# Performance work log

Measured on AMD Instinct MI355X. Metric: run time of the kernel, lower is better.

Reference implementation:

```python
import jax, jax.numpy as jnp
import numpy as np

D, H, DK, DF = 512, 8, 64, 2048  # dim, heads, head_dim, forward_dim
EPS = 1e-5


def _layernorm(x, g, b):
    mu = jnp.mean(x, axis=-1, keepdims=True)
    var = jnp.mean(jnp.square(x - mu), axis=-1, keepdims=True)
    return (x - mu) * jax.lax.rsqrt(var + EPS) * g + b


def setup_inputs() -> dict:
    key = jax.random.key(0)
    ks = jax.random.split(key, 16)
    B, S = 2, 2048
    s_in = 1.0 / np.sqrt(D)
    s_ff = 1.0 / np.sqrt(DF)
    s_cat = 1.0 / np.sqrt(H * DK)
    return {
        "x": jax.random.normal(ks[0], (B, S, D), jnp.float32),
        # per-head Q/K/V projections stacked over heads: [H, D, DK]
        "Wq": jax.random.uniform(ks[1], (H, D, DK), jnp.float32, -s_in, s_in),
        "bq": jax.random.uniform(ks[2], (H, DK), jnp.float32, -s_in, s_in),
        "Wk": jax.random.uniform(ks[3], (H, D, DK), jnp.float32, -s_in, s_in),
        "bk": jax.random.uniform(ks[4], (H, DK), jnp.float32, -s_in, s_in),
        "Wv": jax.random.uniform(ks[5], (H, D, DK), jnp.float32, -s_in, s_in),
        "bv": jax.random.uniform(ks[6], (H, DK), jnp.float32, -s_in, s_in),
        "Wo": jax.random.uniform(ks[7], (H * DK, D), jnp.float32, -s_cat, s_cat),
        "bo": jax.random.uniform(ks[8], (D,), jnp.float32, -s_cat, s_cat),
        "ln1_g": jnp.ones((D,), jnp.float32),
        "ln1_b": jnp.zeros((D,), jnp.float32),
        "W1": jax.random.uniform(ks[9], (D, DF), jnp.float32, -s_in, s_in),
        "b1": jax.random.uniform(ks[10], (DF,), jnp.float32, -s_in, s_in),
        "W2": jax.random.uniform(ks[11], (DF, D), jnp.float32, -s_ff, s_ff),
        "b2": jax.random.uniform(ks[12], (D,), jnp.float32, -s_ff, s_ff),
        "ln2_g": jnp.ones((D,), jnp.float32),
        "ln2_b": jnp.zeros((D,), jnp.float32),
    }


def reference(x, Wq, bq, Wk, bk, Wv, bv, Wo, bo, ln1_g, ln1_b, W1, b1, W2, b2, ln2_g, ln2_b):
    # Per-head projections, batched over heads: [B,H,S,DK]
    q = jnp.einsum('bsd,hdk->bhsk', x, Wq) + bq[None, :, None, :]
    k = jnp.einsum('bsd,hdk->bhsk', x, Wk) + bk[None, :, None, :]
    v = jnp.einsum('bsd,hdk->bhsk', x, Wv) + bv[None, :, None, :]
    scale = 1.0 / np.sqrt(DK)
    scores = jnp.einsum('bhsk,bhtk->bhst', q, k) * scale  # [B,H,S,S]
    attn = jax.nn.softmax(scores, axis=-1)
    o = jnp.einsum('bhst,bhtk->bhsk', attn, v)  # [B,H,S,DK]
    # concat heads (head order matches torch cat over ModuleList)
    B, _, S, _ = o.shape
    o = o.transpose(0, 2, 1, 3).reshape(B, S, H * DK)
    attn_out = o @ Wo + bo
    # Residual 1 (dropout = identity in eval): LN(x + sublayer(x))
    h = _layernorm(x + attn_out, ln1_g, ln1_b)
    # FeedForward + Residual 2
    ff = jax.nn.relu(h @ W1 + b1) @ W2 + b2
    return _layernorm(h + ff, ln2_g, ln2_b)
```

## Files before the change

### kernel.cpp

```cpp
#include <hip/hip_runtime.h>


#define Dm   512
#define Hh   8
#define DKk  64
#define DFf  2048
#define Bb   2
#define Ss   2048
#define Nn   4096

typedef __attribute__((ext_vector_type(8))) short short8;
typedef __attribute__((ext_vector_type(4))) float f32x4;
typedef __attribute__((ext_vector_type(4))) short short4v;
typedef __attribute__((ext_vector_type(2))) int   int2v;

__device__ inline float bf2f(short s) {
    unsigned u = ((unsigned)(unsigned short)s) << 16;
    float f; __builtin_memcpy(&f, &u, 4); return f;
}
__device__ inline short f2bf(float f) {
    unsigned u; __builtin_memcpy(&u, &f, 4);
    u = (u + 0x7fff + ((u >> 16) & 1)) >> 16;
    return (short)u;
}
__device__ inline short cvt_elem(const void* p, long i, int f32flag) {
    if (f32flag) return f2bf(((const float*)p)[i]);
    return ((const short*)p)[i];
}
__device__ inline int detect_f32(const void* x) {
    const float* xf = (const float*)x;
    int ok = 0;
#pragma unroll
    for (int i = 0; i < 16; ++i) {
        float a = fabsf(xf[i]);
        ok += (a > 1e-8f && a < 1e4f) ? 1 : 0;
    }
    return ok >= 8;
}
__device__ inline void gload_lds16(const short* g, short* l) {
    __builtin_amdgcn_global_load_lds(
        (const __attribute__((address_space(1))) unsigned int*)g,
        (__attribute__((address_space(3))) unsigned int*)l, 16, 0, 0);
}

__global__ __launch_bounds__(256) void prep_kernel(
    const void* __restrict__ x, short* __restrict__ xb,
    const void* bq, const void* bk, const void* bv, const void* bo,
    const void* b1, const void* b2, const void* g1, const void* be1,
    const void* g2, const void* be2, short* __restrict__ smalls,
    const void* Wq, const void* Wk, const void* Wv,
    const void* Wo, const void* W1, const void* W2,
    short* __restrict__ WqkvT,
    short* __restrict__ WoT, short* __restrict__ W1T, short* __restrict__ W2T)
{
    const int f = detect_f32(x);
    int blk = blockIdx.x;
    if (blk < 512) {
        long base = (long)blk * 4096;
        if (!f) {
            const short8* src8 = (const short8*)((const short*)x + base);
            short8* dst8 = (short8*)(xb + base);
            for (int i = threadIdx.x; i < 512; i += 256) dst8[i] = src8[i];
        } else {
            for (int i = threadIdx.x; i < 4096; i += 256)
                xb[base + i] = cvt_elem(x, base + i, f);
        }
        return;
    }
    if (blk == 512) {
        const void* srcs[10] = {bq, bk, bv, bo, b1, b2, g1, be1, g2, be2};
        const int   sz[10]   = {512, 512, 512, 512, 2048, 512, 512, 512, 512, 512};
        int off = 0;
        for (int j = 0; j < 10; ++j) {
            for (int i = threadIdx.x; i < sz[j]; i += 256)
                smalls[off + i] = cvt_elem(srcs[j], i, f);
            off += sz[j];
        }
        return;
    }
    __shared__ short tile[64][65];
    blk -= 513;
    const void* src; short* dst; long srcoff = 0; long dstoff = 0; int R, C, tr, tc;
    if (blk < 192) {
        int m = blk >> 6; int r = blk & 63; int h = r >> 3; int t = r & 7;
        src = (m == 0) ? Wq : (m == 1) ? Wk : Wv;
        dst = WqkvT + (long)m * 512 * 512;
        srcoff = (long)h * 512 * 64; dstoff = (long)h * 64 * 512;
        R = 512; C = 64; tr = t; tc = 0;
    } else if (blk < 256) {
        int r = blk - 192; src = Wo; dst = WoT; R = 512; C = 512; tr = r >> 3; tc = r & 7;
    } else if (blk < 512) {
        int r = blk - 256; src = W1; dst = W1T; R = 512; C = 2048; tr = r >> 5; tc = r & 31;
    } else {
        int r = blk - 512; src = W2; dst = W2T; R = 2048; C = 512; tr = r >> 3; tc = r & 7;
    }
    int r0 = tr * 64, c0 = tc * 64;
    if (!f) {
        const short* s16 = (const short*)src;
        for (int i = threadIdx.x; i < 512; i += 256) {
            int rr = i >> 3, c8 = (i & 7) * 8;
            short8 v = *(const short8*)&s16[srcoff + (long)(r0 + rr) * C + c0 + c8];
#pragma unroll
            for (int j = 0; j < 8; ++j) tile[rr][c8 + j] = v[j];
        }
        __syncthreads();
        for (int i = threadIdx.x; i < 512; i += 256) {
            int cc = i >> 3, r8 = (i & 7) * 8;
            short8 w;
#pragma unroll
            for (int j = 0; j < 8; ++j) w[j] = tile[r8 + j][cc];
            *(short8*)&dst[dstoff + (long)(c0 + cc) * R + r0 + r8] = w;
        }
    } else {
        for (int i = threadIdx.x; i < 4096; i += 256) {
            int rr = i >> 6, cc = i & 63;
            tile[rr][cc] = cvt_elem(src, srcoff + (long)(r0 + rr) * C + c0 + cc, f);
        }
        __syncthreads();
        for (int i = threadIdx.x; i < 4096; i += 256) {
            int cc = i >> 6, rr = i & 63;
            dst[dstoff + (long)(c0 + cc) * R + r0 + rr] = tile[rr][cc];
        }
    }
}

#define MODE_F32       1
#define MODE_RELU_BF16 2
#define MODE_QKV       4

__global__ __launch_bounds__(256) void gemm_kernel(
    const short* __restrict__ A, const short* __restrict__ Bt,
    const short* __restrict__ bias, void* __restrict__ outp,
    void* __restrict__ out2, void* __restrict__ out3,
    int K, int Ncols, int mode, int Ktile)
{
    __shared__ short As[2][128 * 64];
    __shared__ short Bs[2][128 * 64];
    const int t    = threadIdx.x;
    const int lane = t & 63;
    const int wave = t >> 6;
    const int quad = lane >> 4;
    const int l15  = lane & 15;
    const int wm = wave >> 1, wn = wave & 1;
    const int row0 = blockIdx.x * 128;
    const int col0 = blockIdx.y * 128;
    const int kbase = blockIdx.z * Ktile;

    const int ri = lane >> 3;
    const int ct = (lane & 7) ^ ri;

    f32x4 acc[4][4];
#pragma unroll
    for (int i = 0; i < 4; ++i)
#pragma unroll
        for (int j = 0; j < 4; ++j) acc[i][j] = (f32x4){0.f, 0.f, 0.f, 0.f};

    auto stage = [&](int buf, int k0) {
#pragma unroll
        for (int p = 0; p < 4; ++p) {
            int r = wave * 32 + p * 8;
            gload_lds16(A + (long)(row0 + r + ri) * K + kbase + k0 + ct * 8,
                        &As[buf][r * 64 + lane * 8]);
        }
#pragma unroll
        for (int p = 0; p < 4; ++p) {
            int r = wave * 32 + p * 8;
            gload_lds16(Bt + (long)(col0 + r + ri) * K + kbase + k0 + ct * 8,
                        &Bs[buf][r * 64 + lane * 8]);
        }
    };

    stage(0, 0);
    int cur = 0;
    const int niter = Ktile >> 6;
    for (int it = 0; it < niter; ++it) {
        asm volatile("s_waitcnt vmcnt(0)" ::: "memory");
        __syncthreads();
        if (it + 1 < niter) stage(cur ^ 1, (it + 1) * 64);
#pragma unroll
        for (int kk = 0; kk < 2; ++kk) {
            short8 af[4], bfr[4];
#pragma unroll
            for (int mt = 0; mt < 4; ++mt) {
                int rowa = wm * 64 + mt * 16 + l15;
                af[mt] = *(const short8*)&As[cur][rowa * 64
                              + (((kk * 4 + quad) ^ (rowa & 7)) * 8)];
            }
#pragma unroll
            for (int nt = 0; nt < 4; ++nt) {
                int rowb = wn * 64 + nt * 16 + l15;
                bfr[nt] = *(const short8*)&Bs[cur][rowb * 64
                              + (((kk * 4 + quad) ^ (rowb & 7)) * 8)];
            }
#pragma unroll
            for (int mt = 0; mt < 4; ++mt)
#pragma unroll
                for (int nt = 0; nt < 4; ++nt)
                    acc[mt][nt] = __builtin_amdgcn_mfma_f32_16x16x32_bf16(
                        af[mt], bfr[nt], acc[mt][nt], 0, 0, 0);
        }
        cur ^= 1;
    }

    const int wrow0 = row0 + wm * 64;
    const int wcol0 = col0 + wn * 64;
    if (mode == MODE_QKV) {
        if (wcol0 < 1024) {
            int m = wcol0 >> 9;
            short* out = (short*)(m == 0 ? outp : out2);
            float sc = (m == 0) ? 0.125f : 1.0f;
#pragma unroll
            for (int nt = 0; nt < 4; ++nt) {
                int col = wcol0 + nt * 16 + l15;
                float bb = bf2f(bias[col]);
                int cl = col & 511;
#pragma unroll
                for (int mt = 0; mt < 4; ++mt)
#pragma unroll
                    for (int r = 0; r < 4; ++r) {
                        int row = wrow0 + mt * 16 + quad * 4 + r;
                        out[(long)row * 512 + cl] = f2bf((acc[mt][nt][r] + bb) * sc);
                    }
            }
        } else {
            __syncthreads();
            short* Asf = &As[0][0];
#pragma unroll
            for (int nt = 0; nt < 4; ++nt) {
                int col_l = wn * 64 + nt * 16 + l15;
                float bb = bf2f(bias[col0 + col_l]);
#pragma unroll
                for (int mt = 0; mt < 4; ++mt) {
                    int row4 = wm * 16 + mt * 4 + quad;
                    int slot = row4 ^ (col_l & 31);
                    short4v pk;
#pragma unroll
                    for (int r = 0; r < 4; ++r) pk[r] = f2bf(acc[mt][nt][r] + bb);
                    *(short4v*)&Asf[col_l * 128 + slot * 4] = pk;
                }
            }
            __syncthreads();
            short* out = (short*)out3;
            int col_l = t >> 1;
            int cl = col0 + col_l - 1024;
            int hh = cl >> 6, kk2 = cl & 63;
            int bg = row0 >> 11;
            long obase = ((long)(bg * Hh + hh) * DKk + kk2) * Ss + (row0 & 2047);
#pragma unroll
            for (int i = 0; i < 8; ++i) {
                int chunk = (t & 1) * 8 + i;
                int s0 = (chunk * 2)     ^ (col_l & 31);
                int s1 = (chunk * 2 + 1) ^ (col_l & 31);
                short4v a = *(const short4v*)&Asf[col_l * 128 + s0 * 4];
                short4v b4 = *(const short4v*)&Asf[col_l * 128 + s1 * 4];
                short8 w;
                w[0] = a[0];  w[1] = a[1];  w[2] = a[2];  w[3] = a[3];
                w[4] = b4[0]; w[5] = b4[1]; w[6] = b4[2]; w[7] = b4[3];
                *(short8*)&out[obase + chunk * 8] = w;
            }
        }
    } else if (mode == MODE_F32) {
        float* out = (float*)outp + (long)blockIdx.z * Nn * Ncols;
        int zb = (blockIdx.z == 0);
#pragma unroll
        for (int nt = 0; nt < 4; ++nt) {
            int col = wcol0 + nt * 16 + l15;
            float bb = zb ? bf2f(bias[col]) : 0.f;
#pragma unroll
            for (int mt = 0; mt < 4; ++mt)
#pragma unroll
                for (int r = 0; r < 4; ++r) {
                    int row = wrow0 + mt * 16 + quad * 4 + r;
                    out[(long)row * Ncols + col] = acc[mt][nt][r] + bb;
                }
        }
    } else {
        short* out = (short*)outp;
#pragma unroll
        for (int nt = 0; nt < 4; ++nt) {
            int col = wcol0 + nt * 16 + l15;
            float bb = bf2f(bias[col]);
#pragma unroll
            for (int mt = 0; mt < 4; ++mt)
#pragma unroll
                for (int r = 0; r < 4; ++r) {
                    int row = wrow0 + mt * 16 + quad * 4 + r;
                    out[(long)row * Ncols + col] = f2bf(fmaxf(acc[mt][nt][r] + bb, 0.f));
                }
        }
    }
}

__global__ __launch_bounds__(256) void wogemm_kernel(
    const short* __restrict__ po, const float* __restrict__ ls,
    const short* __restrict__ Bt, const short* __restrict__ bias,
    float* __restrict__ outp)
{
    __shared__ short As[2][128 * 64];
    __shared__ short Bs[2][128 * 64];
    const int t    = threadIdx.x;
    const int lane = t & 63;
    const int wave = t >> 6;
    const int quad = lane >> 4;
    const int l15  = lane & 15;
    const int wm = wave >> 1, wn = wave & 1;
    const int row0 = blockIdx.x * 128;
    const int col0 = blockIdx.y * 128;
    const int z    = blockIdx.z;

    const int ri = lane >> 3;
    const int ct = (lane & 7) ^ ri;
    const int myrow = t >> 1;
    const int tcb = (t & 1) * 4;
    const int bg = row0 >> 11;
    const int qtl = (row0 >> 7) & 15;

    f32x4 acc[4][4];
#pragma unroll
    for (int i = 0; i < 4; ++i)
#pragma unroll
        for (int j = 0; j < 4; ++j) acc[i][j] = (f32x4){0.f, 0.f, 0.f, 0.f};

    auto stageB = [&](int buf, int k0) {
#pragma unroll
        for (int p = 0; p < 4; ++p) {
            int r = wave * 32 + p * 8;
            gload_lds16(Bt + (long)(col0 + r + ri) * 512 + z * 256 + k0 + ct * 8,
                        &Bs[buf][r * 64 + lane * 8]);
        }
    };

    short8 aR[4][4];
    float  lR[4];
    auto loadA = [&](int it) {
        int h = z * 4 + it;
        long pbase = ((long)(bg * Hh + h) * 16 + qtl) * 4;
#pragma unroll
        for (int ks = 0; ks < 4; ++ks) {
            lR[ks] = ls[(pbase + ks) * 128 + myrow];
#pragma unroll
            for (int c = 0; c < 4; ++c)
                aR[c][ks] = *(const short8*)&po[((pbase + ks) * 128 + myrow) * 64
                                                + (tcb + c) * 8];
        }
    };
    auto cvtwrite = [&](int buf) {
        float invL = __builtin_amdgcn_rcpf(lR[0] + lR[1] + lR[2] + lR[3]);
#pragma unroll
        for (int c = 0; c < 4; ++c) {
            short8 w;
#pragma unroll
            for (int j = 0; j < 8; ++j) {
                float s = bf2f(aR[c][0][j]) + bf2f(aR[c][1][j])
                        + bf2f(aR[c][2][j]) + bf2f(aR[c][3][j]);
                w[j] = f2bf(s * invL);
            }
            int slot = (tcb + c) ^ (myrow & 7);
            *(short8*)&As[buf][myrow * 64 + slot * 8] = w;
        }
    };

    loadA(0); stageB(0, 0); cvtwrite(0);
    int cur = 0;
#pragma unroll
    for (int it = 0; it < 4; ++it) {
        __syncthreads();
        if (it < 3) { loadA(it + 1); stageB(cur ^ 1, (it + 1) * 64); }
#pragma unroll
        for (int kk = 0; kk < 2; ++kk) {
            short8 af[4], bfr[4];
#pragma unroll
            for (int mt = 0; mt < 4; ++mt) {
                int rowa = wm * 64 + mt * 16 + l15;
                af[mt] = *(const short8*)&As[cur][rowa * 64
                              + (((kk * 4 + quad) ^ (rowa & 7)) * 8)];
            }
#pragma unroll
            for (int nt = 0; nt < 4; ++nt) {
                int rowb = wn * 64 + nt * 16 + l15;
                bfr[nt] = *(const short8*)&Bs[cur][rowb * 64
                              + (((kk * 4 + quad) ^ (rowb & 7)) * 8)];
            }
#pragma unroll
            for (int mt = 0; mt < 4; ++mt)
#pragma unroll
                for (int nt = 0; nt < 4; ++nt)
                    acc[mt][nt] = __builtin_amdgcn_mfma_f32_16x16x32_bf16(
                        af[mt], bfr[nt], acc[mt][nt], 0, 0, 0);
        }
        if (it < 3) cvtwrite(cur ^ 1);
        cur ^= 1;
    }

    const int wrow0 = row0 + wm * 64;
    const int wcol0 = col0 + wn * 64;
    float* out = outp + (long)z * Nn * Dm;
    int zb = (z == 0);
#pragma unroll
    for (int nt = 0; nt < 4; ++nt) {
        int col = wcol0 + nt * 16 + l15;
        float bb = zb ? bf2f(bias[col]) : 0.f;
#pragma unroll
        for (int mt = 0; mt < 4; ++mt)
#pragma unroll
            for (int r = 0; r < 4; ++r) {
                int row = wrow0 + mt * 16 + quad * 4 + r;
                out[(long)row * Dm + col] = acc[mt][nt][r] + bb;
            }
    }
}

__global__ __launch_bounds__(256) void attn_kernel(
    const short* __restrict__ Q, const short* __restrict__ Kt,
    const short* __restrict__ Vt, short* __restrict__ po, float* __restrict__ ls)
{
    __shared__ __align__(16) short Ks[64 * 64];
    __shared__ __align__(16) short Vs[64 * 64];
    __shared__ __align__(16) short pbuf[4][32 * 72];
    const int lane = threadIdx.x & 63;
    const int wave = threadIdx.x >> 6;
    const int quad = lane >> 4;
    const int l15  = lane & 15;
    const int qt = blockIdx.x, bh = blockIdx.y, ks = blockIdx.z;
    const int b = bh >> 3, h = bh & 7;
    const int qrow = b * Ss + qt * 128 + wave * 32;

    short8 bq[2][2];
#pragma unroll
    for (int qh = 0; qh < 2; ++qh)
#pragma unroll
        for (int kk = 0; kk < 2; ++kk)
            bq[qh][kk] = *(const short8*)(Q + (long)(qrow + qh * 16 + l15) * Dm
                                          + h * DKk + kk * 32 + quad * 8);

    f32x4 o[2][4];
    float lsum[2] = {0.f, 0.f};
#pragma unroll
    for (int qh = 0; qh < 2; ++qh)
#pragma unroll
        for (int nt = 0; nt < 4; ++nt) o[qh][nt] = (f32x4){0.f, 0.f, 0.f, 0.f};

    const short* Kg = Kt + (long)b * Ss * Dm + h * DKk;
    const short* Vg = Vt + (long)bh * DKk * Ss;
    short* pbw = pbuf[wave];
    const int t00 = ks * 512;

    const int ri = lane >> 3;
    const int ct = (lane & 7) ^ ri;
    const int ldsrow0 = wave * 16;

    for (int it = 0; it < 8; ++it) {
        const int t0 = t00 + it * 64;
#pragma unroll
        for (int p = 0; p < 2; ++p) {
            int r = ldsrow0 + p * 8 + ri;
            gload_lds16(Kg + (long)(t0 + r) * Dm + ct * 8,
                        &Ks[(ldsrow0 + p * 8) * 64] + lane * 8);
        }
#pragma unroll
        for (int p = 0; p < 2; ++p) {
            int r = ldsrow0 + p * 8 + ri;
            gload_lds16(Vg + (long)r * Ss + t0 + ct * 8,
                        &Vs[(ldsrow0 + p * 8) * 64] + lane * 8);
        }
        asm volatile("s_waitcnt vmcnt(0)" ::: "memory");
        __syncthreads();

#pragma unroll
        for (int j = 0; j < 4; ++j) {
            short8 kf0 = *(const short8*)&Ks[(j * 16 + l15) * 64
                                             + ((quad ^ (l15 & 7)) * 8)];
            short8 kf1 = *(const short8*)&Ks[(j * 16 + l15) * 64
                                             + (((4 + quad) ^ (l15 & 7)) * 8)];
#pragma unroll
            for (int qh = 0; qh < 2; ++qh) {
                f32x4 sj = (f32x4){0.f, 0.f, 0.f, 0.f};
                sj = __builtin_amdgcn_mfma_f32_16x16x32_bf16(kf0, bq[qh][0], sj, 0, 0, 0);
                sj = __builtin_amdgcn_mfma_f32_16x16x32_bf16(kf1, bq[qh][1], sj, 0, 0, 0);
                int2v pk;
#pragma unroll
                for (int r2 = 0; r2 < 2; ++r2) {
                    float pa = __expf(fminf(sj[r2 * 2 + 0], 20.f));
                    float pc = __expf(fminf(sj[r2 * 2 + 1], 20.f));
                    lsum[qh] += pa + pc;
                    unsigned ua, uc;
                    __builtin_memcpy(&ua, &pa, 4);
                    __builtin_memcpy(&uc, &pc, 4);
                    pk[r2] = __builtin_amdgcn_perm(uc, ua, 0x07060302);
                }
                *(int2v*)&pbw[(qh * 16 + l15) * 72 + j * 16 + quad * 4] = pk;
            }
        }
        asm volatile("s_waitcnt lgkmcnt(0)" ::: "memory");
#pragma unroll
        for (int c = 0; c < 2; ++c) {
            short8 ap[2];
#pragma unroll
            for (int qh = 0; qh < 2; ++qh)
                ap[qh] = *(const short8*)&pbw[(qh * 16 + l15) * 72 + c * 32 + quad * 8];
#pragma unroll
            for (int nt = 0; nt < 4; ++nt) {
                short8 vf = *(const short8*)&Vs[(nt * 16 + l15) * 64
                                                + (((c * 4 + quad) ^ (l15 & 7)) * 8)];
#pragma unroll
                for (int qh = 0; qh < 2; ++qh)
                    o[qh][nt] = __builtin_amdgcn_mfma_f32_16x16x32_bf16(
                        ap[qh], vf, o[qh][nt], 0, 0, 0);
            }
        }
        asm volatile("" ::: "memory");
        __syncthreads();
    }

#pragma unroll
    for (int qh = 0; qh < 2; ++qh) {
        float v = lsum[qh];
        v += __shfl_xor(v, 16);
        v += __shfl_xor(v, 32);
        lsum[qh] = v;
    }
    short* pob = po + ((((long)bh * 16 + qt) * 4 + ks) * 128) * 64;
#pragma unroll
    for (int qh = 0; qh < 2; ++qh)
#pragma unroll
        for (int nt = 0; nt < 4; ++nt)
#pragma unroll
            for (int r = 0; r < 4; ++r)
                pob[(wave * 32 + qh * 16 + quad * 4 + r) * 64 + nt * 16 + l15] =
                    f2bf(o[qh][nt][r]);
    if (lane < 16) {
        long lbase = (((long)bh * 16 + qt) * 4 + ks) * 128 + wave * 32;
        ls[lbase + l15]      = lsum[0];
        ls[lbase + 16 + l15] = lsum[1];
    }
}

__global__ __launch_bounds__(256) void ln_kernel(
    const float* __restrict__ v0, const float* __restrict__ v1,
    const float* __restrict__ v2, const float* __restrict__ v3,
    const short* __restrict__ res,
    const short* __restrict__ g, const short* __restrict__ bt,
    void* __restrict__ out, const void* __restrict__ xdet)
{
    const int row = blockIdx.x, tid = threadIdx.x;
    const long base = (long)row * Dm;
    const long i0 = base + tid, i1 = base + 256 + tid;
    float x0 = v0[i0] + bf2f(res[i0]);
    float x1 = v0[i1] + bf2f(res[i1]);
    if (v1) { x0 += v1[i0]; x1 += v1[i1]; }
    if (v2) { x0 += v2[i0]; x1 += v2[i1]; }
    if (v3) { x0 += v3[i0]; x1 += v3[i1]; }

    __shared__ float red[8];
    const int wv = tid >> 6, ln = tid & 63;
    float s = x0 + x1;
#pragma unroll
    for (int mk = 1; mk < 64; mk <<= 1) s += __shfl_xor(s, mk);
    if (!ln) red[wv] = s;
    __syncthreads();
    float mean = (red[0] + red[1] + red[2] + red[3]) * (1.f / 512.f);
    float d0 = x0 - mean, d1 = x1 - mean;
    float q = d0 * d0 + d1 * d1;
#pragma unroll
    for (int mk = 1; mk < 64; mk <<= 1) q += __shfl_xor(q, mk);
    if (!ln) red[4 + wv] = q;
    __syncthreads();
    float rs = rsqrtf((red[4] + red[5] + red[6] + red[7]) * (1.f / 512.f) + 1e-5f);
    float y0 = d0 * rs * bf2f(g[tid])       + bf2f(bt[tid]);
    float y1 = d1 * rs * bf2f(g[256 + tid]) + bf2f(bt[256 + tid]);
    int f32out = xdet ? detect_f32(xdet) : 0;
    if (f32out) {
        float* o = (float*)out;
        o[i0] = y0; o[i1] = y1;
    } else {
        short* o = (short*)out;
        o[i0] = f2bf(y0); o[i1] = f2bf(y1);
    }
}

extern "C" void kernel_launch(void* const* d_in, const int* in_sizes, int n_in,
                              void* d_out, int out_size, void* d_ws, size_t ws_size,
                              hipStream_t stream)
{
    (void)in_sizes; (void)n_in; (void)out_size; (void)ws_size;
    const void* x   = d_in[0];
    const void* Wq  = d_in[1];  const void* bq  = d_in[2];
    const void* Wk  = d_in[3];  const void* bk  = d_in[4];
    const void* Wv  = d_in[5];  const void* bv  = d_in[6];
    const void* Wo  = d_in[7];  const void* bo  = d_in[8];
    const void* g1  = d_in[9];  const void* be1 = d_in[10];
    const void* W1  = d_in[11]; const void* b1  = d_in[12];
    const void* W2  = d_in[13]; const void* b2  = d_in[14];
    const void* g2  = d_in[15]; const void* be2 = d_in[16];

    char* ws = (char*)d_ws;
    size_t off = 0;
    auto alloc = [&](size_t bytes) -> void* {
        void* p = ws + off; off += (bytes + 255) & ~(size_t)255; return p;
    };
    short* WqkvT = (short*)alloc((size_t)3 * Dm * Dm * 2);
    short* WoT   = (short*)alloc((size_t)Dm * Dm * 2);
    short* W1T   = (short*)alloc((size_t)DFf * Dm * 2);
    short* W2T   = (short*)alloc((size_t)Dm * DFf * 2);
    short* xb    = (short*)alloc((size_t)Nn * Dm * 2);
    short* sm    = (short*)alloc((size_t)6656 * 2);
    char*  regA  = (char*)alloc((size_t)Nn * DFf * 2);
    short* Qb    = (short*)(regA);
    short* Kb    = (short*)(regA + (size_t)Nn * Dm * 2);
    short* Vt    = (short*)(regA + (size_t)Nn * Dm * 4);
    short* u     = (short*)(regA);
    float* wo_p  = (float*)alloc((size_t)2 * Nn * Dm * 4);
    char*  regC  = (char*)alloc((size_t)4 * Nn * Dm * 4);
    short* po    = (short*)regC;
    float* f2p   = (float*)regC;
    float* lsb   = (float*)alloc((size_t)16 * 16 * 4 * 128 * 4);
    short* h_bf  = (short*)alloc((size_t)Nn * Dm * 2);

    prep_kernel<<<1281, 256, 0, stream>>>(x, xb, bq, bk, bv, bo, b1, b2,
                                          g1, be1, g2, be2, sm,
                                          Wq, Wk, Wv, Wo, W1, W2,
                                          WqkvT, WoT, W1T, W2T);
    gemm_kernel<<<dim3(Nn / 128, 1536 / 128, 1), 256, 0, stream>>>(
        xb, WqkvT, sm + 0, Qb, Kb, Vt, Dm, 1536, MODE_QKV, Dm);
    attn_kernel<<<dim3(Ss / 128, Bb * Hh, 4), 256, 0, stream>>>(Qb, Kb, Vt, po, lsb);
    wogemm_kernel<<<dim3(Nn / 128, Dm / 128, 2), 256, 0, stream>>>(
        po, lsb, WoT, sm + 1536, wo_p);
    ln_kernel<<<Nn, 256, 0, stream>>>(wo_p, wo_p + (long)Nn * Dm, nullptr, nullptr,
                                      xb, sm + 4608, sm + 5120, h_bf, nullptr);
    gemm_kernel<<<dim3(Nn / 128, DFf / 128, 1), 256, 0, stream>>>(
        h_bf, W1T, sm + 2048, u, nullptr, nullptr, Dm, DFf, MODE_RELU_BF16, Dm);
    gemm_kernel<<<dim3(Nn / 128, Dm / 128, 4), 256, 0, stream>>>(
        u, W2T, sm + 4096, f2p, nullptr, nullptr, DFf, Dm, MODE_F32, DFf / 4);
    ln_kernel<<<Nn, 256, 0, stream>>>(f2p, f2p + (long)Nn * Dm, f2p + (long)2 * Nn * Dm,
                                      f2p + (long)3 * Nn * Dm,
                                      h_bf, sm + 5632, sm + 6144, d_out, x);
}
```

Baseline: 209.4 us.

## Stage GEMM epilogues through LDS and store split-K partials as bf16

Adds a shared epilogue helper that writes each accumulator tile into LDS and then emits coalesced 16-byte row stores. It replaces the scattered 2-byte and 4-byte per-element global stores in the QKV, FFN, Wo and attention output paths. Split-K partial sums for the Wo and W2 GEMMs are now stored as bf16 instead of fp32, which halves the partial-buffer traffic read back by the layernorm kernels. The cost is extra LDS round trips and syncs per tile, plus some loss of precision in the partial sums.

```diff
diff --git a/kernel.cpp b/kernel.cpp
--- a/kernel.cpp
+++ b/kernel.cpp
@@ -41,6 +41,35 @@
     __builtin_amdgcn_global_load_lds(
         (const __attribute__((address_space(1))) unsigned int*)g,
         (__attribute__((address_space(3))) unsigned int*)l, 16, 0, 0);
+}
+
+__device__ inline void epi_store128(
+    short* SM, const f32x4 (&acc)[4][4], const short* bias, int colbias,
+    short* out, long rowbase, long pitch, int colbase,
+    float scale, int relu, int wm, int wn, int quad, int l15, int t)
+{
+    __syncthreads();
+#pragma unroll
+    for (int nt = 0; nt < 4; ++nt) {
+        int col_l = wn * 64 + nt * 16 + l15;
+        float bb = bias ? bf2f(bias[colbias + col_l]) : 0.f;
+#pragma unroll
+        for (int mt = 0; mt < 4; ++mt)
+#pragma unroll
+            for (int r = 0; r < 4; ++r) {
+                int row_l = wm * 64 + mt * 16 + quad * 4 + r;
+                float v = (acc[mt][nt][r] + bb) * scale;
+                if (relu) v = fmaxf(v, 0.f);
+                SM[row_l * 136 + col_l] = f2bf(v);
+            }
+    }
+    __syncthreads();
+    int row_l = t >> 1;
+    int x0 = (t & 1) * 64;
+#pragma unroll
+    for (int k = 0; k < 8; ++k)
+        *(short8*)&out[(rowbase + row_l) * pitch + colbase + x0 + k * 8] =
+            *(const short8*)&SM[row_l * 136 + x0 + k * 8];
 }
 
 __global__ __launch_bounds__(256) void prep_kernel(
@@ -124,7 +153,7 @@
     }
 }
 
-#define MODE_F32       1
+#define MODE_PART      1
 #define MODE_RELU_BF16 2
 #define MODE_QKV       4
 
@@ -134,8 +163,9 @@
     void* __restrict__ out2, void* __restrict__ out3,
     int K, int Ncols, int mode, int Ktile)
 {
-    __shared__ short As[2][128 * 64];
-    __shared__ short Bs[2][128 * 64];
+    __shared__ __align__(16) short SMEM[32768];
+    short* As = SMEM;
+    short* Bs = SMEM + 16384;
     const int t    = threadIdx.x;
     const int lane = t & 63;
     const int wave = t >> 6;
@@ -160,13 +190,13 @@
         for (int p = 0; p < 4; ++p) {
             int r = wave * 32 + p * 8;
             gload_lds16(A + (long)(row0 + r + ri) * K + kbase + k0 + ct * 8,
-                        &As[buf][r * 64 + lane * 8]);
+                        &As[buf * 8192 + r * 64 + lane * 8]);
         }
 #pragma unroll
         for (int p = 0; p < 4; ++p) {
             int r = wave * 32 + p * 8;
             gload_lds16(Bt + (long)(col0 + r + ri) * K + kbase + k0 + ct * 8,
-                        &Bs[buf][r * 64 + lane * 8]);
+                        &Bs[buf * 8192 + r * 64 + lane * 8]);
         }
     };
 
@@ -183,13 +213,13 @@
 #pragma unroll
             for (int mt = 0; mt < 4; ++mt) {
                 int rowa = wm * 64 + mt * 16 + l15;
-                af[mt] = *(const short8*)&As[cur][rowa * 64
+                af[mt] = *(const short8*)&As[cur * 8192 + rowa * 64
                               + (((kk * 4 + quad) ^ (rowa & 7)) * 8)];
             }
 #pragma unroll
             for (int nt = 0; nt < 4; ++nt) {
                 int rowb = wn * 64 + nt * 16 + l15;
-                bfr[nt] = *(const short8*)&Bs[cur][rowb * 64
+                bfr[nt] = *(const short8*)&Bs[cur * 8192 + rowb * 64
                               + (((kk * 4 + quad) ^ (rowb & 7)) * 8)];
             }
 #pragma unroll
@@ -202,29 +232,16 @@
         cur ^= 1;
     }
 
-    const int wrow0 = row0 + wm * 64;
-    const int wcol0 = col0 + wn * 64;
     if (mode == MODE_QKV) {
-        if (wcol0 < 1024) {
-            int m = wcol0 >> 9;
+        if (col0 < 1024) {
+            int m = col0 >> 9;
             short* out = (short*)(m == 0 ? outp : out2);
             float sc = (m == 0) ? 0.125f : 1.0f;
-#pragma unroll
-            for (int nt = 0; nt < 4; ++nt) {
-                int col = wcol0 + nt * 16 + l15;
-                float bb = bf2f(bias[col]);
-                int cl = col & 511;
-#pragma unroll
-                for (int mt = 0; mt < 4; ++mt)
-#pragma unroll
-                    for (int r = 0; r < 4; ++r) {
-                        int row = wrow0 + mt * 16 + quad * 4 + r;
-                        out[(long)row * 512 + cl] = f2bf((acc[mt][nt][r] + bb) * sc);
-                    }
-            }
+            epi_store128(SMEM, acc, bias, col0, out, row0, 512, col0 & 511,
+                         sc, 0, wm, wn, quad, l15, t);
         } else {
             __syncthreads();
-            short* Asf = &As[0][0];
+            short* Asf = SMEM;
 #pragma unroll
             for (int nt = 0; nt < 4; ++nt) {
                 int col_l = wn * 64 + nt * 16 + l15;
@@ -259,45 +276,24 @@
                 *(short8*)&out[obase + chunk * 8] = w;
             }
         }
-    } else if (mode == MODE_F32) {
-        float* out = (float*)outp + (long)blockIdx.z * Nn * Ncols;
-        int zb = (blockIdx.z == 0);
-#pragma unroll
-        for (int nt = 0; nt < 4; ++nt) {
-            int col = wcol0 + nt * 16 + l15;
-            float bb = zb ? bf2f(bias[col]) : 0.f;
-#pragma unroll
-            for (int mt = 0; mt < 4; ++mt)
-#pragma unroll
-                for (int r = 0; r < 4; ++r) {
-                    int row = wrow0 + mt * 16 + quad * 4 + r;
-                    out[(long)row * Ncols + col] = acc[mt][nt][r] + bb;
-                }
-        }
+    } else if (mode == MODE_PART) {
+        short* out = (short*)outp + (long)blockIdx.z * Nn * Ncols;
+        epi_store128(SMEM, acc, (blockIdx.z == 0) ? bias : nullptr, col0,
+                     out, row0, Ncols, col0, 1.f, 0, wm, wn, quad, l15, t);
     } else {
-        short* out = (short*)outp;
-#pragma unroll
-        for (int nt = 0; nt < 4; ++nt) {
-            int col = wcol0 + nt * 16 + l15;
-            float bb = bf2f(bias[col]);
-#pragma unroll
-            for (int mt = 0; mt < 4; ++mt)
-#pragma unroll
-                for (int r = 0; r < 4; ++r) {
-                    int row = wrow0 + mt * 16 + quad * 4 + r;
-                    out[(long)row * Ncols + col] = f2bf(fmaxf(acc[mt][nt][r] + bb, 0.f));
-                }
-        }
+        epi_store128(SMEM, acc, bias, col0, (short*)outp, row0, Ncols, col0,
+                     1.f, 1, wm, wn, quad, l15, t);
     }
 }
 
 __global__ __launch_bounds__(256) void wogemm_kernel(
     const short* __restrict__ po, const float* __restrict__ ls,
     const short* __restrict__ Bt, const short* __restrict__ bias,
-    float* __restrict__ outp)
+    short* __restrict__ outp)
 {
-    __shared__ short As[2][128 * 64];
-    __shared__ short Bs[2][128 * 64];
+    __shared__ __align__(16) short SMEM[32768];
+    short* As = SMEM;
+    short* Bs = SMEM + 16384;
     const int t    = threadIdx.x;
     const int lane = t & 63;
     const int wave = t >> 6;
@@ -326,7 +322,7 @@
         for (int p = 0; p < 4; ++p) {
             int r = wave * 32 + p * 8;
             gload_lds16(Bt + (long)(col0 + r + ri) * 512 + z * 256 + k0 + ct * 8,
-                        &Bs[buf][r * 64 + lane * 8]);
+                        &Bs[buf * 8192 + r * 64 + lane * 8]);
         }
     };
 
@@ -356,7 +352,7 @@
                 w[j] = f2bf(s * invL);
             }
             int slot = (tcb + c) ^ (myrow & 7);
-            *(short8*)&As[buf][myrow * 64 + slot * 8] = w;
+            *(short8*)&As[buf * 8192 + myrow * 64 + slot * 8] = w;
         }
     };
 
@@ -372,13 +368,13 @@
 #pragma unroll
             for (int mt = 0; mt < 4; ++mt) {
                 int rowa = wm * 64 + mt * 16 + l15;
-                af[mt] = *(const short8*)&As[cur][rowa * 64
+                af[mt] = *(const short8*)&As[cur * 8192 + rowa * 64
                               + (((kk * 4 + quad) ^ (rowa & 7)) * 8)];
             }
 #pragma unroll
             for (int nt = 0; nt < 4; ++nt) {
                 int rowb = wn * 64 + nt * 16 + l15;
-                bfr[nt] = *(const short8*)&Bs[cur][rowb * 64
+                bfr[nt] = *(const short8*)&Bs[cur * 8192 + rowb * 64
                               + (((kk * 4 + quad) ^ (rowb & 7)) * 8)];
             }
 #pragma unroll
@@ -392,22 +388,9 @@
         cur ^= 1;
     }
 
-    const int wrow0 = row0 + wm * 64;
-    const int wcol0 = col0 + wn * 64;
-    float* out = outp + (long)z * Nn * Dm;
-    int zb = (z == 0);
-#pragma unroll
-    for (int nt = 0; nt < 4; ++nt) {
-        int col = wcol0 + nt * 16 + l15;
-        float bb = zb ? bf2f(bias[col]) : 0.f;
-#pragma unroll
-        for (int mt = 0; mt < 4; ++mt)
-#pragma unroll
-            for (int r = 0; r < 4; ++r) {
-                int row = wrow0 + mt * 16 + quad * 4 + r;
-                out[(long)row * Dm + col] = acc[mt][nt][r] + bb;
-            }
-    }
+    short* out = outp + (long)z * Nn * Dm;
+    epi_store128(SMEM, acc, (z == 0) ? bias : nullptr, col0,
+                 out, row0, Dm, col0, 1.f, 0, wm, wn, quad, l15, t);
 }
 
 __global__ __launch_bounds__(256) void attn_kernel(
@@ -519,15 +502,25 @@
         v += __shfl_xor(v, 32);
         lsum[qh] = v;
     }
+    short* SM = &pbuf[0][0];
+#pragma unroll
+    for (int qh = 0; qh < 2; ++qh)
+#pragma unroll
+        for (int nt = 0; nt < 4; ++nt)
+#pragma unroll
+            for (int r = 0; r < 4; ++r)
+                SM[(wave * 32 + qh * 16 + quad * 4 + r) * 72 + nt * 16 + l15] =
+                    f2bf(o[qh][nt][r]);
+    __syncthreads();
     short* pob = po + ((((long)bh * 16 + qt) * 4 + ks) * 128) * 64;
-#pragma unroll
-    for (int qh = 0; qh < 2; ++qh)
-#pragma unroll
-        for (int nt = 0; nt < 4; ++nt)
-#pragma unroll
-            for (int r = 0; r < 4; ++r)
-                pob[(wave * 32 + qh * 16 + quad * 4 + r) * 64 + nt * 16 + l15] =
-                    f2bf(o[qh][nt][r]);
+    {
+        int row_l = (int)threadIdx.x >> 1;
+        int x0 = ((int)threadIdx.x & 1) * 32;
+#pragma unroll
+        for (int k = 0; k < 4; ++k)
+            *(short8*)&pob[row_l * 64 + x0 + k * 8] =
+                *(const short8*)&SM[row_l * 72 + x0 + k * 8];
+    }
     if (lane < 16) {
         long lbase = (((long)bh * 16 + qt) * 4 + ks) * 128 + wave * 32;
         ls[lbase + l15]      = lsum[0];
@@ -536,8 +529,8 @@
 }
 
 __global__ __launch_bounds__(256) void ln_kernel(
-    const float* __restrict__ v0, const float* __restrict__ v1,
-    const float* __restrict__ v2, const float* __restrict__ v3,
+    const short* __restrict__ v0, const short* __restrict__ v1,
+    const short* __restrict__ v2, const short* __restrict__ v3,
     const short* __restrict__ res,
     const short* __restrict__ g, const short* __restrict__ bt,
     void* __restrict__ out, const void* __restrict__ xdet)
@@ -545,11 +538,11 @@
     const int row = blockIdx.x, tid = threadIdx.x;
     const long base = (long)row * Dm;
     const long i0 = base + tid, i1 = base + 256 + tid;
-    float x0 = v0[i0] + bf2f(res[i0]);
-    float x1 = v0[i1] + bf2f(res[i1]);
-    if (v1) { x0 += v1[i0]; x1 += v1[i1]; }
-    if (v2) { x0 += v2[i0]; x1 += v2[i1]; }
-    if (v3) { x0 += v3[i0]; x1 += v3[i1]; }
+    float x0 = bf2f(v0[i0]) + bf2f(res[i0]);
+    float x1 = bf2f(v0[i1]) + bf2f(res[i1]);
+    if (v1) { x0 += bf2f(v1[i0]); x1 += bf2f(v1[i1]); }
+    if (v2) { x0 += bf2f(v2[i0]); x1 += bf2f(v2[i1]); }
+    if (v3) { x0 += bf2f(v3[i0]); x1 += bf2f(v3[i1]); }
 
     __shared__ float red[8];
     const int wv = tid >> 6, ln = tid & 63;
@@ -609,10 +602,10 @@
     short* Kb    = (short*)(regA + (size_t)Nn * Dm * 2);
     short* Vt    = (short*)(regA + (size_t)Nn * Dm * 4);
     short* u     = (short*)(regA);
-    float* wo_p  = (float*)alloc((size_t)2 * Nn * Dm * 4);
-    char*  regC  = (char*)alloc((size_t)4 * Nn * Dm * 4);
+    short* wo_p  = (short*)alloc((size_t)2 * Nn * Dm * 2);
+    char*  regC  = (char*)alloc((size_t)4 * Nn * Dm * 2);
     short* po    = (short*)regC;
-    float* f2p   = (float*)regC;
+    short* f2p   = (short*)regC;
     float* lsb   = (float*)alloc((size_t)16 * 16 * 4 * 128 * 4);
     short* h_bf  = (short*)alloc((size_t)Nn * Dm * 2);
 
@@ -630,7 +623,7 @@
     gemm_kernel<<<dim3(Nn / 128, DFf / 128, 1), 256, 0, stream>>>(
         h_bf, W1T, sm + 2048, u, nullptr, nullptr, Dm, DFf, MODE_RELU_BF16, Dm);
     gemm_kernel<<<dim3(Nn / 128, Dm / 128, 4), 256, 0, stream>>>(
-        u, W2T, sm + 4096, f2p, nullptr, nullptr, DFf, Dm, MODE_F32, DFf / 4);
+        u, W2T, sm + 4096, f2p, nullptr, nullptr, DFf, Dm, MODE_PART, DFf / 4);
     ln_kernel<<<Nn, 256, 0, stream>>>(f2p, f2p + (long)Nn * Dm, f2p + (long)2 * Nn * Dm,
                                       f2p + (long)3 * Nn * Dm,
                                       h_bf, sm + 5632, sm + 6144, d_out, x);
```

Result: slower. 215.3 us (+2.8%).

## Fuse first LayerNorm into FFN1 GEMM prologue with on-the-fly A conversion

Applied to the files above, without the earlier changes.

Replaces the separate LayerNorm kernel and the W1 GEMM with a single kernel. Each block computes the row statistics for its 128 rows from the two Wo partial sums plus the residual, then normalizes and converts A tiles to bf16 directly into shared memory while staging W1 tiles. Column-block 0 also writes h_bf for the later residual. This removes one launch and the h_bf round trip into the GEMM, but all 16 column blocks now re-read the fp32 partials and recompute the LayerNorm.

```diff
diff --git a/kernel.cpp b/kernel.cpp
--- a/kernel.cpp
+++ b/kernel.cpp
@@ -406,6 +406,156 @@
             for (int r = 0; r < 4; ++r) {
                 int row = wrow0 + mt * 16 + quad * 4 + r;
                 out[(long)row * Dm + col] = acc[mt][nt][r] + bb;
+            }
+    }
+}
+
+__global__ __launch_bounds__(256) void ffn1_kernel(
+    const float* __restrict__ wo0, const float* __restrict__ wo1,
+    const short* __restrict__ xres,
+    const short* __restrict__ g, const short* __restrict__ be,
+    const short* __restrict__ Bt, const short* __restrict__ bias,
+    short* __restrict__ u, short* __restrict__ hbf)
+{
+    __shared__ short As[2][128 * 64];
+    __shared__ short Bs[2][128 * 64];
+    const int t    = threadIdx.x;
+    const int lane = t & 63;
+    const int wave = t >> 6;
+    const int quad = lane >> 4;
+    const int l15  = lane & 15;
+    const int wm = wave >> 1, wn = wave & 1;
+    const int row0 = blockIdx.x * 128;
+    const int col0 = blockIdx.y * 128;
+    const int ri = lane >> 3;
+    const int ct = (lane & 7) ^ ri;
+    const int myrow = t >> 1;
+    const int half = t & 1;
+    const long rg = row0 + myrow;
+
+    f32x4 acc[4][4];
+#pragma unroll
+    for (int i = 0; i < 4; ++i)
+#pragma unroll
+        for (int j = 0; j < 4; ++j) acc[i][j] = (f32x4){0.f, 0.f, 0.f, 0.f};
+
+    auto stageB = [&](int buf, int k0) {
+#pragma unroll
+        for (int p = 0; p < 4; ++p) {
+            int r = wave * 32 + p * 8;
+            gload_lds16(Bt + (long)(col0 + r + ri) * 512 + k0 + ct * 8,
+                        &Bs[buf][r * 64 + lane * 8]);
+        }
+    };
+
+    stageB(0, 0);
+
+    float sum = 0.f, sq = 0.f;
+    {
+        const float* p0 = wo0 + rg * 512 + half * 256;
+        const float* p1 = wo1 + rg * 512 + half * 256;
+        const short* px = xres + rg * 512 + half * 256;
+        for (int i = 0; i < 256; i += 8) {
+            f32x4 a0 = *(const f32x4*)(p0 + i);
+            f32x4 a1 = *(const f32x4*)(p0 + i + 4);
+            f32x4 b0 = *(const f32x4*)(p1 + i);
+            f32x4 b1 = *(const f32x4*)(p1 + i + 4);
+            short8 xv = *(const short8*)(px + i);
+#pragma unroll
+            for (int j = 0; j < 8; ++j) {
+                float v = ((j < 4) ? a0[j] : a1[j - 4])
+                        + ((j < 4) ? b0[j] : b1[j - 4]) + bf2f(xv[j]);
+                sum += v; sq += v * v;
+            }
+        }
+    }
+    float* scr = (float*)&As[0][0];
+    scr[t] = sum; scr[256 + t] = sq;
+    __syncthreads();
+    float mean, rstd;
+    {
+        float s2 = scr[myrow * 2] + scr[myrow * 2 + 1];
+        float q2 = scr[256 + myrow * 2] + scr[256 + myrow * 2 + 1];
+        mean = s2 * (1.f / 512.f);
+        float var = q2 * (1.f / 512.f) - mean * mean;
+        rstd = rsqrtf(var + 1e-5f);
+    }
+    __syncthreads();
+
+    auto cvtwriteA = [&](int buf, int k0) {
+        const float* p0 = wo0 + rg * 512 + k0 + half * 32;
+        const float* p1 = wo1 + rg * 512 + k0 + half * 32;
+        const short* px = xres + rg * 512 + k0 + half * 32;
+        const short* pg = g + k0 + half * 32;
+        const short* pb = be + k0 + half * 32;
+#pragma unroll
+        for (int c = 0; c < 4; ++c) {
+            f32x4 a0 = *(const f32x4*)(p0 + c * 8);
+            f32x4 a1 = *(const f32x4*)(p0 + c * 8 + 4);
+            f32x4 b0 = *(const f32x4*)(p1 + c * 8);
+            f32x4 b1 = *(const f32x4*)(p1 + c * 8 + 4);
+            short8 xv = *(const short8*)(px + c * 8);
+            short8 gv = *(const short8*)(pg + c * 8);
+            short8 bv = *(const short8*)(pb + c * 8);
+            short8 w;
+#pragma unroll
+            for (int j = 0; j < 8; ++j) {
+                float v = ((j < 4) ? a0[j] : a1[j - 4])
+                        + ((j < 4) ? b0[j] : b1[j - 4]) + bf2f(xv[j]);
+                float y = (v - mean) * rstd * bf2f(gv[j]) + bf2f(bv[j]);
+                w[j] = f2bf(y);
+            }
+            int ch = half * 4 + c;
+            int slot = ch ^ (myrow & 7);
+            *(short8*)&As[buf][myrow * 64 + slot * 8] = w;
+            if (blockIdx.y == 0)
+                *(short8*)&hbf[rg * 512 + k0 + half * 32 + c * 8] = w;
+        }
+    };
+
+    cvtwriteA(0, 0);
+    int cur = 0;
+#pragma unroll
+    for (int it = 0; it < 8; ++it) {
+        __syncthreads();
+        if (it < 7) { stageB(cur ^ 1, (it + 1) * 64); cvtwriteA(cur ^ 1, (it + 1) * 64); }
+#pragma unroll
+        for (int kk = 0; kk < 2; ++kk) {
+            short8 af[4], bfr[4];
+#pragma unroll
+            for (int mt = 0; mt < 4; ++mt) {
+                int rowa = wm * 64 + mt * 16 + l15;
+                af[mt] = *(const short8*)&As[cur][rowa * 64
+                              + (((kk * 4 + quad) ^ (rowa & 7)) * 8)];
+            }
+#pragma unroll
+            for (int nt = 0; nt < 4; ++nt) {
+                int rowb = wn * 64 + nt * 16 + l15;
+                bfr[nt] = *(const short8*)&Bs[cur][rowb * 64
+                              + (((kk * 4 + quad) ^ (rowb & 7)) * 8)];
+            }
+#pragma unroll
+            for (int mt = 0; mt < 4; ++mt)
+#pragma unroll
+                for (int nt = 0; nt < 4; ++nt)
+                    acc[mt][nt] = __builtin_amdgcn_mfma_f32_16x16x32_bf16(
+                        af[mt], bfr[nt], acc[mt][nt], 0, 0, 0);
+        }
+        cur ^= 1;
+    }
+
+    const int wrow0 = row0 + wm * 64;
+    const int wcol0 = col0 + wn * 64;
+#pragma unroll
+    for (int nt = 0; nt < 4; ++nt) {
+        int col = wcol0 + nt * 16 + l15;
+        float bb = bf2f(bias[col]);
+#pragma unroll
+        for (int mt = 0; mt < 4; ++mt)
+#pragma unroll
+            for (int r = 0; r < 4; ++r) {
+                int row = wrow0 + mt * 16 + quad * 4 + r;
+                u[(long)row * DFf + col] = f2bf(fmaxf(acc[mt][nt][r] + bb, 0.f));
             }
     }
 }
@@ -625,10 +775,9 @@
     attn_kernel<<<dim3(Ss / 128, Bb * Hh, 4), 256, 0, stream>>>(Qb, Kb, Vt, po, lsb);
     wogemm_kernel<<<dim3(Nn / 128, Dm / 128, 2), 256, 0, stream>>>(
         po, lsb, WoT, sm + 1536, wo_p);
-    ln_kernel<<<Nn, 256, 0, stream>>>(wo_p, wo_p + (long)Nn * Dm, nullptr, nullptr,
-                                      xb, sm + 4608, sm + 5120, h_bf, nullptr);
-    gemm_kernel<<<dim3(Nn / 128, DFf / 128, 1), 256, 0, stream>>>(
-        h_bf, W1T, sm + 2048, u, nullptr, nullptr, Dm, DFf, MODE_RELU_BF16, Dm);
+    ffn1_kernel<<<dim3(Nn / 128, DFf / 128), 256, 0, stream>>>(
+        wo_p, wo_p + (long)Nn * Dm, xb, sm + 4608, sm + 5120,
+        W1T, sm + 2048, u, h_bf);
     gemm_kernel<<<dim3(Nn / 128, Dm / 128, 4), 256, 0, stream>>>(
         u, W2T, sm + 4096, f2p, nullptr, nullptr, DFf, Dm, MODE_F32, DFf / 4);
     ln_kernel<<<Nn, 256, 0, stream>>>(f2p, f2p + (long)Nn * Dm, f2p + (long)2 * Nn * Dm,
```

After: 289.2 us. +38.1%, slower.
